# Kernel tuning notes

Hardware: AMD Instinct MI355X
Metric: run time of the kernel (lower is better)

## Reference

```python
import jax, jax.numpy as jnp
import numpy as np

ALPHA = 0.2      # LeakyReLU negative slope
NEG_INF = -9e15  # mask fill value from the original


def setup_inputs() -> dict:
    key = jax.random.key(0)
    ks = jax.random.split(key, 6)
    B, N, C, E = 2, 1024, 32, 32  # in_channels == embed_dim (required by bias add)
    x = jax.random.normal(ks[0], (B, N, C), dtype=jnp.float32)
    adj = jax.random.randint(ks[1], (B, N, N), 0, 2, dtype=jnp.int32)
    W1 = jax.random.normal(ks[2], (C, E), dtype=jnp.float32) * 0.1
    W2 = jax.random.normal(ks[3], (2 * C, E), dtype=jnp.float32) * 0.1
    a = jax.random.normal(ks[4], (E, 1), dtype=jnp.float32) * 0.1
    bias = jax.random.normal(ks[5], (E,), dtype=jnp.float32) * 0.1
    return {"x": x, "adj": adj, "W1": W1, "W2": W2, "a": a, "bias": bias}


def reference(x, adj, W1, W2, a, bias):
    B, N, C = x.shape
    # dead code in the original (hidden is never used) -- W1 gets zero grad
    _hidden = jnp.matmul(x, W1)
    # faithful replication of the original's (buggy but deterministic) layout:
    # cat along the flattened pair axis, then view as (B, N, N, 2C)
    rep_chunks = jnp.repeat(x, N, axis=1)       # (B, N*N, C): row k -> x[k//N]
    rep_alt = jnp.tile(x, (1, N, 1))            # (B, N*N, C): row k -> x[k%N]
    all_comb = jnp.concatenate([rep_chunks, rep_alt], axis=1).reshape(B, N, N, 2 * C)
    wx = jnp.einsum('bijc,ce->bije', all_comb, W2)          # (B,N,N,E)
    attn = jax.nn.leaky_relu(wx, negative_slope=ALPHA)
    scores = jnp.einsum('bije,eo->bijo', attn, a)[..., 0]   # (B,N,N)
    scores = jnp.where(adj > 0, scores, NEG_INF)
    attention = jax.nn.softmax(scores, axis=-1)             # dropout: identity (eval)
    out = jnp.matmul(attention, x) + bias                   # (B,N,C), C == E
    return jnp.tanh(out)
```

## Files before the change

### kernel.cpp

```cpp
#include <hip/hip_runtime.h>
#include <math.h>

#define ALPHA 0.2f

constexpr int N = 1024;
constexpr int C = 32;

__global__ __launch_bounds__(256) void uvexp_kernel(
    const float* __restrict__ x, const float* __restrict__ W2,
    const float* __restrict__ a, float* __restrict__ eu, float* __restrict__ ev)
{
    __shared__ float sW2[64 * 32];
    __shared__ float sa[32];
    const int tid = threadIdx.x;
    for (int idx = tid; idx < 64 * 32; idx += 256) sW2[idx] = W2[idx];
    if (tid < 32) sa[tid] = a[tid];
    __syncthreads();

    const int gout = (blockIdx.x * 256 + tid) >> 5;
    const int e = tid & 31;
    const int isV = gout >> 11;
    const int idx = gout & 2047;
    const int b = idx >> 10;
    const int n = idx & 1023;
    const float* xb = x + b * (N * C);

    float acc = 0.f;
    if (!isV) {
        const float* xr = xb + n * 32;
        #pragma unroll
        for (int c = 0; c < 32; ++c) {
            const float xv = xr[c];
            acc = fmaf(xv, sW2[c * 32 + e], acc);
            acc = fmaf(xv, sW2[(c + 32) * 32 + e], acc);
        }
    } else {
        const float* x0 = xb + ((2 * n) & 1023) * 32;
        const float* x1 = xb + ((2 * n + 1) & 1023) * 32;
        #pragma unroll
        for (int c = 0; c < 32; ++c) {
            acc = fmaf(x0[c], sW2[c * 32 + e], acc);
            acc = fmaf(x1[c], sW2[(c + 32) * 32 + e], acc);
        }
    }
    float t = (acc > 0.f ? acc : ALPHA * acc) * sa[e];
    #pragma unroll
    for (int m = 16; m >= 1; m >>= 1) t += __shfl_xor(t, m);
    if (e == 0) (isV ? ev : eu)[idx] = expf(t);
}

__global__ __launch_bounds__(256) void attn_kernel(
    const float* __restrict__ x, const int* __restrict__ adj,
    const float* __restrict__ eu, const float* __restrict__ ev,
    const float* __restrict__ bias, float* __restrict__ out)
{
    __shared__ float sw[1024];
    __shared__ float part[32][33];
    __shared__ float wsumArr[32];

    const int tid = threadIdx.x;
    const int row = blockIdx.x;
    const int b = row >> 10;
    const int i = row & 1023;

    const int4 av = ((const int4*)(adj + (size_t)row * 1024))[tid];
    float w0, w1, w2, w3;
    if (i < 512) {
        const float su = eu[(b << 10) + 2 * i + (tid >= 128 ? 1 : 0)];
        w0 = w1 = w2 = w3 = su;
    } else {
        const float4 vv = ((const float4*)(ev + (b << 10)))[tid];
        w0 = vv.x; w1 = vv.y; w2 = vv.z; w3 = vv.w;
    }
    float4 wv;
    wv.x = av.x > 0 ? w0 : 0.f;
    wv.y = av.y > 0 ? w1 : 0.f;
    wv.z = av.z > 0 ? w2 : 0.f;
    wv.w = av.w > 0 ? w3 : 0.f;
    ((float4*)sw)[tid] = wv;
    __syncthreads();

    const float4* x4 = (const float4*)(x + b * (N * C));
    const int c4 = tid & 7;
    const int jg = tid >> 3;
    float4 acc = make_float4(0.f, 0.f, 0.f, 0.f);
    float wsum = 0.f;
    #pragma unroll 8
    for (int q = 0; q < 32; ++q) {
        const int j = jg * 32 + ((q + jg) & 31);
        const float w = sw[j];
        const float4 xv = x4[j * 8 + c4];
        acc.x = fmaf(w, xv.x, acc.x);
        acc.y = fmaf(w, xv.y, acc.y);
        acc.z = fmaf(w, xv.z, acc.z);
        acc.w = fmaf(w, xv.w, acc.w);
        wsum += w;
    }
    part[jg][c4 * 4 + 0] = acc.x;
    part[jg][c4 * 4 + 1] = acc.y;
    part[jg][c4 * 4 + 2] = acc.z;
    part[jg][c4 * 4 + 3] = acc.w;
    if (c4 == 0) wsumArr[jg] = wsum;
    __syncthreads();

    if (tid < 32) {
        float o = 0.f;
        #pragma unroll
        for (int g = 0; g < 32; ++g) o += part[g][tid];
        float dn = wsumArr[tid];
        #pragma unroll
        for (int m = 16; m >= 1; m >>= 1) dn += __shfl_xor(dn, m);
        if (dn == 0.f) {
            o = 0.f;
            for (int j = 0; j < 1024; ++j) o += x[b * (N * C) + j * 32 + tid];
            dn = 1024.f;
        }
        out[(size_t)row * 32 + tid] = tanhf(fmaf(o, 1.0f / dn, bias[tid]));
    }
}

extern "C" void kernel_launch(void* const* d_in, const int* in_sizes, int n_in,
                              void* d_out, int out_size, void* d_ws, size_t ws_size,
                              hipStream_t stream) {
    const float* x    = (const float*)d_in[0];
    const int*   adj  = (const int*)d_in[1];
    const float* W2   = (const float*)d_in[3];
    const float* a    = (const float*)d_in[4];
    const float* bias = (const float*)d_in[5];
    float* out = (float*)d_out;

    float* eu = (float*)d_ws;
    float* ev = eu + 2 * 1024;

    uvexp_kernel<<<512, 256, 0, stream>>>(x, W2, a, eu, ev);
    attn_kernel<<<2 * 1024, 256, 0, stream>>>(x, adj, eu, ev, bias, out);
}
```

Measured before the change: 82.92 us.

## Process four attention rows per block to reuse x loads across rows

The attention kernel now handles four consecutive rows per block (512 blocks instead of 2048). It stores transposed per-row weights as float4 in shared memory, so each x load feeds four rows' accumulators. The cross-group reduction now uses wave shuffles instead of a shared-memory partial array, and the weight sums are computed up front. This cuts x traffic and block count, at the cost of more registers, fewer blocks, and scalar rather than int4 adjacency loads.

Measured after the change: 78.41 us. -5.4%, faster.

```diff
diff --git a/kernel.cpp b/kernel.cpp
--- a/kernel.cpp
+++ b/kernel.cpp
@@ -49,73 +49,120 @@
     if (e == 0) (isV ? ev : eu)[idx] = expf(t);
 }
 
-__global__ __launch_bounds__(256) void attn_kernel(
+__global__ __launch_bounds__(256) void attn_kernel4(
     const float* __restrict__ x, const int* __restrict__ adj,
     const float* __restrict__ eu, const float* __restrict__ ev,
     const float* __restrict__ bias, float* __restrict__ out)
 {
-    __shared__ float sw[1024];
-    __shared__ float part[32][33];
-    __shared__ float wsumArr[32];
+    __shared__ float swT[1024 * 4];
+    __shared__ float partF[4 * 4 * 32];
+    __shared__ float wsred[4 * 4];
 
     const int tid = threadIdx.x;
-    const int row = blockIdx.x;
-    const int b = row >> 10;
-    const int i = row & 1023;
+    const int row0 = blockIdx.x * 4;
+    const int b = row0 >> 10;
+    const int i0 = row0 & 1023;
+    const int wave = tid >> 6;
+    const int lane = tid & 63;
 
-    const int4 av = ((const int4*)(adj + (size_t)row * 1024))[tid];
-    float w0, w1, w2, w3;
-    if (i < 512) {
-        const float su = eu[(b << 10) + 2 * i + (tid >= 128 ? 1 : 0)];
-        w0 = w1 = w2 = w3 = su;
+    float w[4][4];
+    if (i0 < 512) {
+        float su[4][2];
+        #pragma unroll
+        for (int r = 0; r < 4; ++r) {
+            su[r][0] = eu[(b << 10) + 2 * (i0 + r)];
+            su[r][1] = eu[(b << 10) + 2 * (i0 + r) + 1];
+        }
+        #pragma unroll
+        for (int m = 0; m < 4; ++m) {
+            const int half = m >> 1;
+            #pragma unroll
+            for (int r = 0; r < 4; ++r) {
+                const int aij = adj[(size_t)(row0 + r) * 1024 + tid + 256 * m];
+                w[m][r] = aij > 0 ? su[r][half] : 0.f;
+            }
+        }
     } else {
-        const float4 vv = ((const float4*)(ev + (b << 10)))[tid];
-        w0 = vv.x; w1 = vv.y; w2 = vv.z; w3 = vv.w;
+        #pragma unroll
+        for (int m = 0; m < 4; ++m) {
+            const float evj = ev[(b << 10) + tid + 256 * m];
+            #pragma unroll
+            for (int r = 0; r < 4; ++r) {
+                const int aij = adj[(size_t)(row0 + r) * 1024 + tid + 256 * m];
+                w[m][r] = aij > 0 ? evj : 0.f;
+            }
+        }
     }
-    float4 wv;
-    wv.x = av.x > 0 ? w0 : 0.f;
-    wv.y = av.y > 0 ? w1 : 0.f;
-    wv.z = av.z > 0 ? w2 : 0.f;
-    wv.w = av.w > 0 ? w3 : 0.f;
-    ((float4*)sw)[tid] = wv;
+    float ws[4];
+    #pragma unroll
+    for (int r = 0; r < 4; ++r)
+        ws[r] = (w[0][r] + w[1][r]) + (w[2][r] + w[3][r]);
+    #pragma unroll
+    for (int m = 0; m < 4; ++m)
+        ((float4*)swT)[tid + 256 * m] = make_float4(w[m][0], w[m][1], w[m][2], w[m][3]);
+    #pragma unroll
+    for (int s = 32; s >= 1; s >>= 1) {
+        ws[0] += __shfl_xor(ws[0], s);
+        ws[1] += __shfl_xor(ws[1], s);
+        ws[2] += __shfl_xor(ws[2], s);
+        ws[3] += __shfl_xor(ws[3], s);
+    }
+    if (lane == 0) {
+        #pragma unroll
+        for (int r = 0; r < 4; ++r) wsred[wave * 4 + r] = ws[r];
+    }
     __syncthreads();
 
     const float4* x4 = (const float4*)(x + b * (N * C));
     const int c4 = tid & 7;
     const int jg = tid >> 3;
-    float4 acc = make_float4(0.f, 0.f, 0.f, 0.f);
-    float wsum = 0.f;
+    float4 a0 = make_float4(0.f, 0.f, 0.f, 0.f);
+    float4 a1 = a0, a2 = a0, a3 = a0;
     #pragma unroll 8
     for (int q = 0; q < 32; ++q) {
         const int j = jg * 32 + ((q + jg) & 31);
-        const float w = sw[j];
+        const float4 wv = ((const float4*)swT)[j];
         const float4 xv = x4[j * 8 + c4];
-        acc.x = fmaf(w, xv.x, acc.x);
-        acc.y = fmaf(w, xv.y, acc.y);
-        acc.z = fmaf(w, xv.z, acc.z);
-        acc.w = fmaf(w, xv.w, acc.w);
-        wsum += w;
+        a0.x = fmaf(wv.x, xv.x, a0.x); a0.y = fmaf(wv.x, xv.y, a0.y);
+        a0.z = fmaf(wv.x, xv.z, a0.z); a0.w = fmaf(wv.x, xv.w, a0.w);
+        a1.x = fmaf(wv.y, xv.x, a1.x); a1.y = fmaf(wv.y, xv.y, a1.y);
+        a1.z = fmaf(wv.y, xv.z, a1.z); a1.w = fmaf(wv.y, xv.w, a1.w);
+        a2.x = fmaf(wv.z, xv.x, a2.x); a2.y = fmaf(wv.z, xv.y, a2.y);
+        a2.z = fmaf(wv.z, xv.z, a2.z); a2.w = fmaf(wv.z, xv.w, a2.w);
+        a3.x = fmaf(wv.w, xv.x, a3.x); a3.y = fmaf(wv.w, xv.y, a3.y);
+        a3.z = fmaf(wv.w, xv.z, a3.z); a3.w = fmaf(wv.w, xv.w, a3.w);
     }
-    part[jg][c4 * 4 + 0] = acc.x;
-    part[jg][c4 * 4 + 1] = acc.y;
-    part[jg][c4 * 4 + 2] = acc.z;
-    part[jg][c4 * 4 + 3] = acc.w;
-    if (c4 == 0) wsumArr[jg] = wsum;
+    #pragma unroll
+    for (int s = 8; s <= 32; s <<= 1) {
+        a0.x += __shfl_xor(a0.x, s); a0.y += __shfl_xor(a0.y, s);
+        a0.z += __shfl_xor(a0.z, s); a0.w += __shfl_xor(a0.w, s);
+        a1.x += __shfl_xor(a1.x, s); a1.y += __shfl_xor(a1.y, s);
+        a1.z += __shfl_xor(a1.z, s); a1.w += __shfl_xor(a1.w, s);
+        a2.x += __shfl_xor(a2.x, s); a2.y += __shfl_xor(a2.y, s);
+        a2.z += __shfl_xor(a2.z, s); a2.w += __shfl_xor(a2.w, s);
+        a3.x += __shfl_xor(a3.x, s); a3.y += __shfl_xor(a3.y, s);
+        a3.z += __shfl_xor(a3.z, s); a3.w += __shfl_xor(a3.w, s);
+    }
+    if (lane < 8) {
+        ((float4*)partF)[(wave * 4 + 0) * 8 + c4] = a0;
+        ((float4*)partF)[(wave * 4 + 1) * 8 + c4] = a1;
+        ((float4*)partF)[(wave * 4 + 2) * 8 + c4] = a2;
+        ((float4*)partF)[(wave * 4 + 3) * 8 + c4] = a3;
+    }
     __syncthreads();
 
-    if (tid < 32) {
-        float o = 0.f;
-        #pragma unroll
-        for (int g = 0; g < 32; ++g) o += part[g][tid];
-        float dn = wsumArr[tid];
-        #pragma unroll
-        for (int m = 16; m >= 1; m >>= 1) dn += __shfl_xor(dn, m);
+    if (tid < 128) {
+        const int r = tid >> 5, c = tid & 31;
+        float o = (partF[(0 * 4 + r) * 32 + c] + partF[(1 * 4 + r) * 32 + c]) +
+                  (partF[(2 * 4 + r) * 32 + c] + partF[(3 * 4 + r) * 32 + c]);
+        float dn = (wsred[0 * 4 + r] + wsred[1 * 4 + r]) +
+                   (wsred[2 * 4 + r] + wsred[3 * 4 + r]);
         if (dn == 0.f) {
             o = 0.f;
-            for (int j = 0; j < 1024; ++j) o += x[b * (N * C) + j * 32 + tid];
+            for (int j = 0; j < 1024; ++j) o += x[b * (N * C) + j * 32 + c];
             dn = 1024.f;
         }
-        out[(size_t)row * 32 + tid] = tanhf(fmaf(o, 1.0f / dn, bias[tid]));
+        out[(size_t)(row0 + r) * 32 + c] = tanhf(fmaf(o, 1.0f / dn, bias[c]));
     }
 }
 
@@ -133,5 +180,5 @@
     float* ev = eu + 2 * 1024;
 
     uvexp_kernel<<<512, 256, 0, stream>>>(x, W2, a, eu, ev);
-    attn_kernel<<<2 * 1024, 256, 0, stream>>>(x, adj, eu, ev, bias, out);
+    attn_kernel4<<<512, 256, 0, stream>>>(x, adj, eu, ev, bias, out);
 }
```
